# Performance work log

Hardware: AMD Instinct MI355X
Metric: run time of the kernel (lower is better)

Reference implementation:

```python
import jax, jax.numpy as jnp
import numpy as np

B, T, C = 2, 4096, 512
P, PS, CS, MB, FD = 64, 16, 5, 128, 128


def setup_inputs() -> dict:
    key = jax.random.key(0)
    ks = jax.random.split(key, 9)
    y = jax.random.normal(ks[0], (B, T, C), jnp.float32)
    # per-timestep random patch indices into the sequence axis, sorted per patch
    patches = jnp.sort(jax.random.randint(ks[1], (T, P, PS), 0, T), axis=-1).astype(jnp.int32)
    patches_proj = jax.random.randint(ks[2], (T, P), 0, T).astype(jnp.int32)
    W_BASE = jax.random.normal(ks[3], (P, PS, CS), jnp.float32) * 0.05
    W_BIAS = jax.random.normal(ks[4], (P,), jnp.float32) * 0.05
    W_proj2 = jax.random.normal(ks[5], (C, MB), jnp.float32) * (1.0 / np.sqrt(C).astype(np.float32))
    W_proj_comp = jax.random.normal(ks[6], (C, CS), jnp.float32) * (1.0 / np.sqrt(C).astype(np.float32))
    W_presoftmax1 = jax.random.normal(ks[7], (P, P), jnp.float32) * (1.0 / np.sqrt(P).astype(np.float32))
    W_FINAL = jax.random.normal(ks[8], (MB, FD), jnp.float32) * (1.0 / np.sqrt(MB).astype(np.float32))
    return {
        'y': y,
        'W_BASE': W_BASE,
        'W_BIAS': W_BIAS,
        'W_proj2': W_proj2,
        'W_proj_comp': W_proj_comp,
        'W_presoftmax1': W_presoftmax1,
        'W_FINAL': W_FINAL,
        'patches': patches,
        'patches_proj': patches_proj,
    }


def reference(y, W_BASE, W_BIAS, W_proj2, W_proj_comp, W_presoftmax1, W_FINAL, patches, patches_proj):
    # value branch: project then gather one sequence element per (t, patch)
    bm = jnp.einsum('btc,cm->btm', y, W_proj2)          # [B,T,MB]
    mbg = bm[:, patches_proj, :]                        # [B,T,P,MB]  (MBMB)
    # score branch: compress, gather PS elements per (t, patch), weighted reduce
    yc = jnp.einsum('btc,ck->btk', y, W_proj_comp)      # [B,T,CS]
    g = yc[:, patches, :]                               # [B,T,P,PS,CS]
    res = jnp.einsum('btpsc,psc->btp', g, W_BASE) + W_BIAS   # [B,T,P]
    mix = jnp.einsum('btp,pq->btq', res, W_presoftmax1)      # [B,T,P] (no softmax in source)
    out = jnp.einsum('btp,btpm->btm', mix, mbg)              # [B,T,MB]
    return jnp.einsum('btm,mf->btf', out, W_FINAL)           # [B,T,FD]
```

## Files before the change

kernel.cpp:

```cpp
#include <hip/hip_runtime.h>
#include <hip/hip_bf16.h>

#define B_ 2
#define T_ 4096
#define C_ 512
#define P_ 64
#define PS_ 16
#define CS_ 5
#define MB_ 128
#define FD_ 128

using f32x4 = __attribute__((ext_vector_type(4))) float;
using s16x8 = __attribute__((ext_vector_type(8))) short;
using i32x4 = __attribute__((ext_vector_type(4))) int;

static __device__ __forceinline__ float bf_lo(unsigned u) {
  return __uint_as_float(u << 16);
}
static __device__ __forceinline__ float bf_hi(unsigned u) {
  return __uint_as_float(u & 0xffff0000u);
}
static __device__ __forceinline__ float rdlane_f(float v, int p) {
  return __uint_as_float((unsigned)__builtin_amdgcn_readlane((int)__float_as_uint(v), p));
}
static __device__ __forceinline__ ushort bf16u(float f) {
  unsigned x = __float_as_uint(f);
  unsigned r = (x + 0x7fffu + ((x >> 16) & 1u)) >> 16;
  return (ushort)r;
}

__global__ __launch_bounds__(256) void k_prep(const float* __restrict__ y,
                                              const float* __restrict__ Wc,
                                              const float* __restrict__ Wp2,
                                              const float* __restrict__ WF,
                                              const float* __restrict__ WB,
                                              ushort* __restrict__ ycp,
                                              ushort* __restrict__ Wp2T,
                                              ushort* __restrict__ WFT,
                                              ushort* __restrict__ WBb) {
  const int bx = blockIdx.x;
  const int tid = threadIdx.x;
  if (bx >= 256) {
    for (int id = (bx - 256) * 256 + tid; id < 87040; id += 64 * 256) {
      if (id < 65536) {
        const int c = id >> 7, m = id & 127;
        Wp2T[(size_t)m * C_ + c] = bf16u(Wp2[id]);
      } else if (id < 81920) {
        const int i2 = id - 65536;
        const int m = i2 >> 7, f = i2 & 127;
        WFT[(size_t)f * MB_ + m] = bf16u(WF[i2]);
      } else {
        const int i3 = id - 81920;
        WBb[i3] = bf16u(WB[i3]);
      }
    }
    return;
  }
  const int lane = tid & 63;
  const int wid  = tid >> 6;
  float wc[40];
  {
    const float4* src = (const float4*)(Wc + lane * 40);
    #pragma unroll
    for (int j = 0; j < 10; j++) {
      float4 v = src[j];
      wc[j*4+0] = v.x; wc[j*4+1] = v.y; wc[j*4+2] = v.z; wc[j*4+3] = v.w;
    }
  }
  const int row_base = (bx * 4 + wid) * 8;
  #pragma unroll 2
  for (int r = 0; r < 8; r++) {
    const int row = row_base + r;
    const float4* yr = (const float4*)(y + (size_t)row * C_ + lane * 8);
    float4 a = yr[0], b4 = yr[1];
    float e[8] = {a.x, a.y, a.z, a.w, b4.x, b4.y, b4.z, b4.w};
    float s0 = 0.f, s1 = 0.f, s2 = 0.f, s3 = 0.f, s4 = 0.f;
    #pragma unroll
    for (int j = 0; j < 8; j++) {
      s0 = fmaf(e[j], wc[j*5+0], s0);
      s1 = fmaf(e[j], wc[j*5+1], s1);
      s2 = fmaf(e[j], wc[j*5+2], s2);
      s3 = fmaf(e[j], wc[j*5+3], s3);
      s4 = fmaf(e[j], wc[j*5+4], s4);
    }
    #pragma unroll
    for (int off = 1; off < 64; off <<= 1) {
      s0 += __shfl_xor(s0, off); s1 += __shfl_xor(s1, off);
      s2 += __shfl_xor(s2, off); s3 += __shfl_xor(s3, off);
      s4 += __shfl_xor(s4, off);
    }
    float myv = (lane == 0) ? s0 : (lane == 1) ? s1 : (lane == 2) ? s2
              : (lane == 3) ? s3 : (lane == 4) ? s4 : 0.f;
    if (lane < 8) ycp[(size_t)row * 8 + lane] = bf16u(myv);
  }
}

template<int KTOT, bool OUTBF, bool A_F32>
__global__ __launch_bounds__(256) void k_gemm(const void* __restrict__ Asrc,
                                              const ushort* __restrict__ Bt,
                                              void* __restrict__ Cout) {
  __shared__ __align__(16) char smem[(32 + 64) * 128];
  const int tid  = threadIdx.x;
  const int lane = tid & 63;
  const int wid  = tid >> 6;
  const int wm = wid >> 1, wn = wid & 1;
  const int rowA0 = (blockIdx.x >> 1) * 32;
  const int bn    = blockIdx.x & 1;

  f32x4 acc[2];
  acc[0] = (f32x4){0.f, 0.f, 0.f, 0.f};
  acc[1] = (f32x4){0.f, 0.f, 0.f, 0.f};

  for (int step = 0; step < KTOT / 64; step++) {
    const int kc = step * 64;
    uint4 ra;
    {
      const int r = tid >> 3, sl = tid & 7;
      if (A_F32) {
        const float4* ap = (const float4*)((const float*)Asrc +
                            (size_t)(rowA0 + r) * KTOT + kc + sl * 8);
        float4 f0 = ap[0], f1 = ap[1];
        union { ushort us[8]; uint4 q; } pk;
        pk.us[0] = bf16u(f0.x); pk.us[1] = bf16u(f0.y);
        pk.us[2] = bf16u(f0.z); pk.us[3] = bf16u(f0.w);
        pk.us[4] = bf16u(f1.x); pk.us[5] = bf16u(f1.y);
        pk.us[6] = bf16u(f1.z); pk.us[7] = bf16u(f1.w);
        ra = pk.q;
      } else {
        ra = *(const uint4*)((const ushort*)Asrc +
                             (size_t)(rowA0 + r) * KTOT + kc + sl * 8);
      }
    }
    uint4 rb[2];
    #pragma unroll
    for (int i = 0; i < 2; i++) {
      const int slot = tid + i * 256, r = slot >> 3, sl = slot & 7;
      rb[i] = *(const uint4*)(Bt + (size_t)(bn * 64 + r) * KTOT + kc + sl * 8);
    }
    __syncthreads();
    {
      const int r = tid >> 3, sl = tid & 7;
      *(uint4*)(smem + r * 128 + ((sl * 16) ^ ((r & 7) << 4))) = ra;
    }
    #pragma unroll
    for (int i = 0; i < 2; i++) {
      const int slot = tid + i * 256, r = slot >> 3, sl = slot & 7;
      *(uint4*)(smem + 4096 + r * 128 + ((sl * 16) ^ ((r & 7) << 4))) = rb[i];
    }
    __syncthreads();
    #pragma unroll
    for (int kk = 0; kk < 2; kk++) {
      const int cb = kk * 64 + (lane >> 4) * 16;
      const int r = wm * 16 + (lane & 15);
      s16x8 a = *(const s16x8*)(smem + r * 128 + (cb ^ ((r & 7) << 4)));
      #pragma unroll
      for (int n = 0; n < 2; n++) {
        const int rn = wn * 32 + n * 16 + (lane & 15);
        s16x8 b = *(const s16x8*)(smem + 4096 + rn * 128 + (cb ^ ((rn & 7) << 4)));
        acc[n] = __builtin_amdgcn_mfma_f32_16x16x32_bf16(a, b, acc[n], 0, 0, 0);
      }
    }
  }
  #pragma unroll
  for (int n = 0; n < 2; n++) {
    #pragma unroll
    for (int reg = 0; reg < 4; reg++) {
      const int grow = rowA0 + wm * 16 + (lane >> 4) * 4 + reg;
      const int gcol = bn * 64 + wn * 32 + n * 16 + (lane & 15);
      if (OUTBF)
        ((ushort*)Cout)[(size_t)grow * 128 + gcol] = bf16u(acc[n][reg]);
      else
        ((float*)Cout)[(size_t)grow * 128 + gcol] = acc[n][reg];
    }
  }
}

__global__ __launch_bounds__(256, 4) void k_mid(
    const ushort* __restrict__ ycp,
    const ushort* __restrict__ bmb,
    const ushort* __restrict__ WBb,
    const float* __restrict__ Wbias,
    const float* __restrict__ Wps1,
    const int* __restrict__ patches,
    const int* __restrict__ pproj,
    ushort* __restrict__ obmb)
{
  __shared__ __align__(16) float wps[64 * 64];
  const int tid  = threadIdx.x;
  const int lane = tid & 63;
  const int wid  = tid >> 6;
  const int b    = blockIdx.x >> 10;
  const int t    = (blockIdx.x & 1023) * 4 + wid;

  for (int j = tid; j < 1024; j += 256)
    ((float4*)wps)[j] = ((const float4*)Wps1)[j];
  __syncthreads();

  union { unsigned u[40]; uint4 q[10]; } wbu;
  {
    const uint4* src = (const uint4*)(WBb + lane * 80);
    #pragma unroll
    for (int j = 0; j < 10; j++) wbu.q[j] = src[j];
  }
  const float bias = Wbias[lane];

  int idx[16];
  {
    const i32x4* psrc = (const i32x4*)(patches + (size_t)t * P_ * PS_ + lane * PS_);
    #pragma unroll
    for (int j = 0; j < 4; j++) {
      i32x4 v = __builtin_nontemporal_load(psrc + j);
      idx[j*4+0] = v.x; idx[j*4+1] = v.y; idx[j*4+2] = v.z; idx[j*4+3] = v.w;
    }
  }
  const int pp = __builtin_nontemporal_load(pproj + (size_t)t * P_ + lane);

  const ushort* yb = ycp + (size_t)b * T_ * 8;
  float c0 = bias, c1 = 0.f, c2 = 0.f, c3 = 0.f, c4 = 0.f;
  #pragma unroll
  for (int s = 0; s < 16; s++) {
    uint4 g = *(const uint4*)(yb + (size_t)idx[s] * 8);
    const int e = s * 5;
    const float w0 = ((e+0)&1) ? bf_hi(wbu.u[(e+0)>>1]) : bf_lo(wbu.u[(e+0)>>1]);
    const float w1 = ((e+1)&1) ? bf_hi(wbu.u[(e+1)>>1]) : bf_lo(wbu.u[(e+1)>>1]);
    const float w2 = ((e+2)&1) ? bf_hi(wbu.u[(e+2)>>1]) : bf_lo(wbu.u[(e+2)>>1]);
    const float w3 = ((e+3)&1) ? bf_hi(wbu.u[(e+3)>>1]) : bf_lo(wbu.u[(e+3)>>1]);
    const float w4 = ((e+4)&1) ? bf_hi(wbu.u[(e+4)>>1]) : bf_lo(wbu.u[(e+4)>>1]);
    c0 = fmaf(bf_lo(g.x), w0, c0);
    c1 = fmaf(bf_hi(g.x), w1, c1);
    c2 = fmaf(bf_lo(g.y), w2, c2);
    c3 = fmaf(bf_hi(g.y), w3, c3);
    c4 = fmaf(bf_lo(g.z), w4, c4);
  }
  const float sum = (c0 + c1) + (c2 + c3) + c4;
  float m0 = 0.f, m1 = 0.f, m2 = 0.f, m3 = 0.f;
  #pragma unroll
  for (int p = 0; p < 64; p += 4) {
    m0 = fmaf(rdlane_f(sum, p + 0), wps[(p + 0) * 64 + lane], m0);
    m1 = fmaf(rdlane_f(sum, p + 1), wps[(p + 1) * 64 + lane], m1);
    m2 = fmaf(rdlane_f(sum, p + 2), wps[(p + 2) * 64 + lane], m2);
    m3 = fmaf(rdlane_f(sum, p + 3), wps[(p + 3) * 64 + lane], m3);
  }
  const float mix = (m0 + m1) + (m2 + m3);
  const ushort* bb = bmb + (size_t)b * T_ * MB_;
  float oxa = 0.f, oya = 0.f, oxb = 0.f, oyb = 0.f;
  #pragma unroll
  for (int p = 0; p < 64; p += 2) {
    const float mpa = rdlane_f(mix, p);
    const int rowa = __builtin_amdgcn_readlane(pp, p);
    unsigned va = *(const unsigned*)(bb + (size_t)rowa * MB_ + lane * 2);
    oxa = fmaf(bf_lo(va), mpa, oxa);
    oya = fmaf(bf_hi(va), mpa, oya);
    const float mpb = rdlane_f(mix, p + 1);
    const int rowb = __builtin_amdgcn_readlane(pp, p + 1);
    unsigned vb = *(const unsigned*)(bb + (size_t)rowb * MB_ + lane * 2);
    oxb = fmaf(bf_lo(vb), mpb, oxb);
    oyb = fmaf(bf_hi(vb), mpb, oyb);
  }
  unsigned pkd = (unsigned)bf16u(oxa + oxb) | ((unsigned)bf16u(oya + oyb) << 16);
  __builtin_nontemporal_store(pkd,
      (unsigned*)(obmb + ((size_t)b * T_ + t) * MB_ + lane * 2));
}

extern "C" void kernel_launch(void* const* d_in, const int* in_sizes, int n_in,
                              void* d_out, int out_size, void* d_ws, size_t ws_size,
                              hipStream_t stream) {
  const float* y     = (const float*)d_in[0];
  const float* WB    = (const float*)d_in[1];
  const float* Wbias = (const float*)d_in[2];
  const float* Wp2   = (const float*)d_in[3];
  const float* Wpc   = (const float*)d_in[4];
  const float* Wps1  = (const float*)d_in[5];
  const float* WF    = (const float*)d_in[6];
  const int* patches = (const int*)d_in[7];
  const int* pproj   = (const int*)d_in[8];
  float* out = (float*)d_out;

  char* ws = (char*)d_ws;
  ushort* bmb  = (ushort*)(ws);
  ushort* obmb = (ushort*)(ws + 2097152);
  ushort* ycp  = (ushort*)(ws + 4194304);
  ushort* Wp2T = (ushort*)(ws + 4325376);
  ushort* WFT  = (ushort*)(ws + 4456448);
  ushort* WBb  = (ushort*)(ws + 4489216);

  k_prep<<<dim3(320), dim3(256), 0, stream>>>(y, Wpc, Wp2, WF, WB,
                                              ycp, Wp2T, WFT, WBb);
  k_gemm<512, true,  true ><<<dim3(512), dim3(256), 0, stream>>>((const void*)y, Wp2T, (void*)bmb);
  k_mid <<<dim3(2048), dim3(256), 0, stream>>>(ycp, bmb, WBb, Wbias, Wps1,
                                               patches, pproj, obmb);
  k_gemm<128, false, false><<<dim3(512), dim3(256), 0, stream>>>((const void*)obmb, WFT, (void*)out);
}
```

Measured before the change: 178.0 us.

## Fold compress projection into bf16 MFMA GEMM via extended weight columns

The separate k_prep pass that computed y·W_proj_comp with fp32 FMAs and shuffle reductions is removed. Instead, W_proj_comp is appended as extra padded columns to the transposed W_proj2 weight, so the main GEMM computes both outputs in a third column tile of 64. This avoids re-reading y a second time but computes the compressed projection from bf16-rounded y with 59 wasted columns. The change also reorders block indexing in the GEMM and k_mid and raises k_mid's occupancy hint to 8 blocks per CU.

Measured after the change: 235.4 us. 32.3% more time.

```diff
diff --git a/kernel.cpp b/kernel.cpp
--- a/kernel.cpp
+++ b/kernel.cpp
@@ -29,83 +29,43 @@
   return (ushort)r;
 }
 
-__global__ __launch_bounds__(256) void k_prep(const float* __restrict__ y,
-                                              const float* __restrict__ Wc,
-                                              const float* __restrict__ Wp2,
-                                              const float* __restrict__ WF,
-                                              const float* __restrict__ WB,
-                                              ushort* __restrict__ ycp,
-                                              ushort* __restrict__ Wp2T,
-                                              ushort* __restrict__ WFT,
-                                              ushort* __restrict__ WBb) {
-  const int bx = blockIdx.x;
-  const int tid = threadIdx.x;
-  if (bx >= 256) {
-    for (int id = (bx - 256) * 256 + tid; id < 87040; id += 64 * 256) {
-      if (id < 65536) {
-        const int c = id >> 7, m = id & 127;
-        Wp2T[(size_t)m * C_ + c] = bf16u(Wp2[id]);
-      } else if (id < 81920) {
-        const int i2 = id - 65536;
-        const int m = i2 >> 7, f = i2 & 127;
-        WFT[(size_t)f * MB_ + m] = bf16u(WF[i2]);
-      } else {
-        const int i3 = id - 81920;
-        WBb[i3] = bf16u(WB[i3]);
-      }
-    }
-    return;
-  }
-  const int lane = tid & 63;
-  const int wid  = tid >> 6;
-  float wc[40];
-  {
-    const float4* src = (const float4*)(Wc + lane * 40);
-    #pragma unroll
-    for (int j = 0; j < 10; j++) {
-      float4 v = src[j];
-      wc[j*4+0] = v.x; wc[j*4+1] = v.y; wc[j*4+2] = v.z; wc[j*4+3] = v.w;
-    }
-  }
-  const int row_base = (bx * 4 + wid) * 8;
-  #pragma unroll 2
-  for (int r = 0; r < 8; r++) {
-    const int row = row_base + r;
-    const float4* yr = (const float4*)(y + (size_t)row * C_ + lane * 8);
-    float4 a = yr[0], b4 = yr[1];
-    float e[8] = {a.x, a.y, a.z, a.w, b4.x, b4.y, b4.z, b4.w};
-    float s0 = 0.f, s1 = 0.f, s2 = 0.f, s3 = 0.f, s4 = 0.f;
-    #pragma unroll
-    for (int j = 0; j < 8; j++) {
-      s0 = fmaf(e[j], wc[j*5+0], s0);
-      s1 = fmaf(e[j], wc[j*5+1], s1);
-      s2 = fmaf(e[j], wc[j*5+2], s2);
-      s3 = fmaf(e[j], wc[j*5+3], s3);
-      s4 = fmaf(e[j], wc[j*5+4], s4);
-    }
-    #pragma unroll
-    for (int off = 1; off < 64; off <<= 1) {
-      s0 += __shfl_xor(s0, off); s1 += __shfl_xor(s1, off);
-      s2 += __shfl_xor(s2, off); s3 += __shfl_xor(s3, off);
-      s4 += __shfl_xor(s4, off);
-    }
-    float myv = (lane == 0) ? s0 : (lane == 1) ? s1 : (lane == 2) ? s2
-              : (lane == 3) ? s3 : (lane == 4) ? s4 : 0.f;
-    if (lane < 8) ycp[(size_t)row * 8 + lane] = bf16u(myv);
-  }
-}
-
-template<int KTOT, bool OUTBF, bool A_F32>
+__global__ __launch_bounds__(256) void k_prepW(const float* __restrict__ Wp2,
+                                               const float* __restrict__ Wpc,
+                                               const float* __restrict__ WF,
+                                               const float* __restrict__ WB,
+                                               ushort* __restrict__ BtExt,
+                                               ushort* __restrict__ WFT,
+                                               ushort* __restrict__ WBb) {
+  for (int id = blockIdx.x * 256 + threadIdx.x; id < 119808; id += 128 * 256) {
+    if (id < 98304) {
+      const int row = id >> 9, c = id & 511;
+      float v = 0.f;
+      if (row < 128)       v = Wp2[(size_t)c * MB_ + row];
+      else if (row < 133)  v = Wpc[(size_t)c * CS_ + (row - 128)];
+      BtExt[id] = bf16u(v);
+    } else if (id < 114688) {
+      const int i2 = id - 98304;
+      const int m = i2 >> 7, f = i2 & 127;
+      WFT[(size_t)f * MB_ + m] = bf16u(WF[i2]);
+    } else {
+      const int i3 = id - 114688;
+      WBb[i3] = bf16u(WB[i3]);
+    }
+  }
+}
+
+template<int KTOT, int MODE, bool A_F32>
 __global__ __launch_bounds__(256) void k_gemm(const void* __restrict__ Asrc,
                                               const ushort* __restrict__ Bt,
-                                              void* __restrict__ Cout) {
+                                              void* __restrict__ Cout,
+                                              ushort* __restrict__ ycp) {
   __shared__ __align__(16) char smem[(32 + 64) * 128];
   const int tid  = threadIdx.x;
   const int lane = tid & 63;
   const int wid  = tid >> 6;
   const int wm = wid >> 1, wn = wid & 1;
-  const int rowA0 = (blockIdx.x >> 1) * 32;
-  const int bn    = blockIdx.x & 1;
+  const int rowA0 = (blockIdx.x & 255) * 32;
+  const int bn    = blockIdx.x >> 8;
 
   f32x4 acc[2];
   acc[0] = (f32x4){0.f, 0.f, 0.f, 0.f};
@@ -166,16 +126,24 @@
     #pragma unroll
     for (int reg = 0; reg < 4; reg++) {
       const int grow = rowA0 + wm * 16 + (lane >> 4) * 4 + reg;
-      const int gcol = bn * 64 + wn * 32 + n * 16 + (lane & 15);
-      if (OUTBF)
-        ((ushort*)Cout)[(size_t)grow * 128 + gcol] = bf16u(acc[n][reg]);
-      else
-        ((float*)Cout)[(size_t)grow * 128 + gcol] = acc[n][reg];
-    }
-  }
-}
-
-__global__ __launch_bounds__(256, 4) void k_mid(
+      const int col  = bn * 64 + wn * 32 + n * 16 + (lane & 15);
+      if (MODE == 0) {
+        ((float*)Cout)[(size_t)grow * 128 + col] = acc[n][reg];
+      } else if (MODE == 1) {
+        ((ushort*)Cout)[(size_t)grow * 128 + col] = bf16u(acc[n][reg]);
+      } else {
+        if (bn < 2) {
+          ((ushort*)Cout)[(size_t)grow * 128 + col] = bf16u(acc[n][reg]);
+        } else {
+          const int c = col - 128;
+          if (c < 5) ycp[(size_t)grow * 8 + c] = bf16u(acc[n][reg]);
+        }
+      }
+    }
+  }
+}
+
+__global__ __launch_bounds__(256, 8) void k_mid(
     const ushort* __restrict__ ycp,
     const ushort* __restrict__ bmb,
     const ushort* __restrict__ WBb,
@@ -189,8 +157,10 @@
   const int tid  = threadIdx.x;
   const int lane = tid & 63;
   const int wid  = tid >> 6;
-  const int b    = blockIdx.x >> 10;
-  const int t    = (blockIdx.x & 1023) * 4 + wid;
+  const int bid  = blockIdx.x;
+  const int b    = (bid >> 2) & 1;
+  const int g    = ((bid >> 3) << 2) | (bid & 3);
+  const int t    = g * 4 + wid;
 
   for (int j = tid; j < 1024; j += 256)
     ((float4*)wps)[j] = ((const float4*)Wps1)[j];
@@ -219,18 +189,18 @@
   float c0 = bias, c1 = 0.f, c2 = 0.f, c3 = 0.f, c4 = 0.f;
   #pragma unroll
   for (int s = 0; s < 16; s++) {
-    uint4 g = *(const uint4*)(yb + (size_t)idx[s] * 8);
+    uint4 g4 = *(const uint4*)(yb + (size_t)idx[s] * 8);
     const int e = s * 5;
     const float w0 = ((e+0)&1) ? bf_hi(wbu.u[(e+0)>>1]) : bf_lo(wbu.u[(e+0)>>1]);
     const float w1 = ((e+1)&1) ? bf_hi(wbu.u[(e+1)>>1]) : bf_lo(wbu.u[(e+1)>>1]);
     const float w2 = ((e+2)&1) ? bf_hi(wbu.u[(e+2)>>1]) : bf_lo(wbu.u[(e+2)>>1]);
     const float w3 = ((e+3)&1) ? bf_hi(wbu.u[(e+3)>>1]) : bf_lo(wbu.u[(e+3)>>1]);
     const float w4 = ((e+4)&1) ? bf_hi(wbu.u[(e+4)>>1]) : bf_lo(wbu.u[(e+4)>>1]);
-    c0 = fmaf(bf_lo(g.x), w0, c0);
-    c1 = fmaf(bf_hi(g.x), w1, c1);
-    c2 = fmaf(bf_lo(g.y), w2, c2);
-    c3 = fmaf(bf_hi(g.y), w3, c3);
-    c4 = fmaf(bf_lo(g.z), w4, c4);
+    c0 = fmaf(bf_lo(g4.x), w0, c0);
+    c1 = fmaf(bf_hi(g4.x), w1, c1);
+    c2 = fmaf(bf_lo(g4.y), w2, c2);
+    c3 = fmaf(bf_hi(g4.y), w3, c3);
+    c4 = fmaf(bf_lo(g4.z), w4, c4);
   }
   const float sum = (c0 + c1) + (c2 + c3) + c4;
   float m0 = 0.f, m1 = 0.f, m2 = 0.f, m3 = 0.f;
@@ -277,17 +247,19 @@
   float* out = (float*)d_out;
 
   char* ws = (char*)d_ws;
-  ushort* bmb  = (ushort*)(ws);
-  ushort* obmb = (ushort*)(ws + 2097152);
-  ushort* ycp  = (ushort*)(ws + 4194304);
-  ushort* Wp2T = (ushort*)(ws + 4325376);
-  ushort* WFT  = (ushort*)(ws + 4456448);
-  ushort* WBb  = (ushort*)(ws + 4489216);
-
-  k_prep<<<dim3(320), dim3(256), 0, stream>>>(y, Wpc, Wp2, WF, WB,
-                                              ycp, Wp2T, WFT, WBb);
-  k_gemm<512, true,  true ><<<dim3(512), dim3(256), 0, stream>>>((const void*)y, Wp2T, (void*)bmb);
+  ushort* bmb   = (ushort*)(ws);
+  ushort* obmb  = (ushort*)(ws + 2097152);
+  ushort* ycp   = (ushort*)(ws + 4194304);
+  ushort* BtExt = (ushort*)(ws + 4325376);
+  ushort* WFT   = (ushort*)(ws + 4521984);
+  ushort* WBb   = (ushort*)(ws + 4554752);
+
+  k_prepW<<<dim3(128), dim3(256), 0, stream>>>(Wp2, Wpc, WF, WB,
+                                               BtExt, WFT, WBb);
+  k_gemm<512, 2, true ><<<dim3(768), dim3(256), 0, stream>>>(
+      (const void*)y, BtExt, (void*)bmb, ycp);
   k_mid <<<dim3(2048), dim3(256), 0, stream>>>(ycp, bmb, WBb, Wbias, Wps1,
                                                patches, pproj, obmb);
-  k_gemm<128, false, false><<<dim3(512), dim3(256), 0, stream>>>((const void*)obmb, WFT, (void*)out);
-}
+  k_gemm<128, 0, false><<<dim3(512), dim3(256), 0, stream>>>(
+      (const void*)obmb, WFT, (void*)out, nullptr);
+}
```
